# Kernel optimization log

Hardware: AMD Instinct MI355X
Metric: run time of the kernel (lower is better)

Reference implementation:

```python
import jax, jax.numpy as jnp
import numpy as np

B, N, E = 64, 1024, 16384  # graphs, nodes per graph, edges per graph
N_ITER = 5
NORMALIZE = True
NUM_INIT_LABELS = 16


def _unique_inverse(h):
    """Equivalent of torch.unique(h, sorted=True, return_inverse=True)[1] for 1-D h."""
    order = jnp.argsort(h)
    sh = h[order]
    bnd = jnp.concatenate([jnp.zeros(1, jnp.int32), (sh[1:] != sh[:-1]).astype(jnp.int32)])
    ranks = jnp.cumsum(bnd)  # dense rank in sorted-unique order
    return jnp.zeros_like(ranks).at[order].set(ranks)


def _wl_iteration(mask, labels, hash_w):
    """One WL iteration for all graphs.
    mask: [B,N,N] bool dense adjacency (sparse-to-dense, as in the torch code)
    labels: [B,N] int32
    hash_w: [2] float32 (Linear(2,1,bias=False) weight)
    Returns new labels [B,N] int32.
    """
    w0, w1 = hash_w[0], hash_w[1]
    lab_f = labels.astype(jnp.float32)
    deg = mask.sum(-1).astype(jnp.float32)                      # [B,N] valid-neighbor count
    K = deg.max(axis=-1, keepdims=True)                         # per-graph max_neighbors
    # sum of neighbor labels (gather+reduce over the dense mask, memory-bound)
    seg = jnp.einsum('bij,bj->bi', mask.astype(jnp.float32), lab_f)  # [B,N]
    # torch builds [N,max_neighbors] rows: node label in col 0-feature, sorted
    # neighbor labels (padded with -1) in col 1-feature, hashes each pair with
    # w0*node + w1*neigh and sums over columns. Closed form (sort is sum-invariant):
    #   K*w0*node + w1*(sum_neighbors - (K - deg))
    hashed = K * w0 * lab_f + w1 * (seg + deg - K)              # [B,N]
    return jax.vmap(_unique_inverse)(hashed)


def setup_inputs() -> dict:
    key = jax.random.key(0)
    k1, k2, k3, k4 = jax.random.split(key, 4)
    edge_src = jax.random.randint(k1, (B, E), 0, N, dtype=jnp.int32)
    edge_dst = jax.random.randint(k2, (B, E), 0, N, dtype=jnp.int32)
    labels = jax.random.randint(k3, (B, N), 0, NUM_INIT_LABELS, dtype=jnp.int32)
    hash_w = jax.random.normal(k4, (2,), dtype=jnp.float32)
    return {"edge_src": edge_src, "edge_dst": edge_dst, "labels": labels, "hash_w": hash_w}


def reference(edge_src, edge_dst, labels, hash_w):
    # sparse-to-dense neighbor mask, as in the torch module
    b_idx = jnp.arange(B, dtype=jnp.int32)[:, None]
    mask = jnp.zeros((B, N, N), dtype=bool).at[b_idx, edge_src, edge_dst].set(True)

    all_labels = [labels]
    for _ in range(N_ITER):
        all_labels.append(_wl_iteration(mask, all_labels[-1], hash_w))

    # feature vectors: per graph, bincount of labels summed over all iterations.
    # Labels are always < N (unique-inverse ranks < N; initial labels < 16),
    # so N bins is a tight static upper bound for torch's max_label+1; the extra
    # zero columns do not change the Gram matrix.
    labels_all = jnp.stack(all_labels, axis=1).reshape(B, -1)   # [B, (n_iter+1)*N]
    feats = jax.vmap(lambda l: jnp.zeros((N,), jnp.float32).at[l].add(1.0))(labels_all)

    kernel = feats @ feats.T                                    # [B,B]
    if NORMALIZE:
        d = jnp.sqrt(jnp.diag(kernel))
        kernel = kernel / (d[None, :] * d[:, None])
    return kernel
```

## Files before the change

### kernel.cpp

```cpp
#include <hip/hip_runtime.h>

#define B 64
#define N 1024
#define E 16384
#define WPR 32
#define NITER 5
#define CSR_SLOTS (E + N)
#define MAXP 20

#define FEATS_OFF 0
#define DIAG_OFF  ((size_t)B * N * 4)

__global__ void __launch_bounds__(1024) wl_mega_k(const int* __restrict__ src,
                                                  const int* __restrict__ dstp,
                                                  const int* __restrict__ lab0,
                                                  const float* __restrict__ hw,
                                                  unsigned int* __restrict__ feats,
                                                  float* __restrict__ diag) {
    __shared__ union {
        unsigned int chunk[N * WPR];
        struct {
            unsigned short nbr[CSR_SLOTS];
            struct {
                int hist[N];
                int scan[N];
                float grp[N];
                int flag[N];
            } pb;
            int meta[N];
            unsigned short perm[N];
            int dh[256];
            int dtop[256];
        } s;
    } u;
    __shared__ int s_lab[N + 2];
    __shared__ unsigned int s_feats[N];
    __shared__ int s_wsum[16];
    __shared__ int s_kp[16];
    __shared__ float s_mn[16], s_mx[16];
    __shared__ int s_anytie;
    int b = blockIdx.x, t = threadIdx.x;
    int lane = t & 63, w = t >> 6;

    const int* sg = src + (size_t)b * E;
    const int* dg_ = dstp + (size_t)b * E;
    int es[16], ed[16];
#pragma unroll
    for (int k = 0; k < 16; ++k) {
        es[k] = sg[t + k * 1024];
        ed[k] = dg_[t + k * 1024];
    }
    int l0 = lab0[(size_t)b * N + t];
    float w0 = hw[0], w1 = hw[1];
#pragma unroll
    for (int k = 0; k < 8; ++k)
        ((uint4*)u.chunk)[t + k * 1024] = make_uint4(0, 0, 0, 0);
    s_lab[t] = l0;
    s_feats[t] = 0;
    if (t == 0) { s_lab[N] = 0; s_anytie = 0; }
    __syncthreads();
#pragma unroll
    for (int v = 0; v < 16; ++v) {
        unsigned long long m = __ballot(l0 == v);
        if (lane == v) {
            int c = __popcll(m);
            if (c) atomicAdd(&s_feats[v], (unsigned)c);
        }
    }

#pragma unroll
    for (int k = 0; k < 16; ++k) {
        int wlog = ed[k] >> 5;
        int g = wlog >> 2;
        int p = (g + es[k]) & 7;
        atomicOr(&u.chunk[es[k] * WPR + p * 4 + (wlog & 3)], 1u << (ed[k] & 31));
    }
    __syncthreads();
    uint4 r[8];
    {
        const uint4* row4 = (const uint4*)(u.chunk + t * WPR);
#pragma unroll
        for (int g = 0; g < 8; ++g)
            r[g] = row4[(g + t) & 7];
    }
    __syncthreads();

    int dg = 0;
#pragma unroll
    for (int k = 0; k < 8; ++k)
        dg += __popc(r[k].x) + __popc(r[k].y) + __popc(r[k].z) + __popc(r[k].w);
    int alloc = (dg + 1) & ~1;

    int f = alloc;
#pragma unroll
    for (int d2 = 1; d2 < 64; d2 <<= 1) {
        int v = __shfl_up(f, d2);
        if (lane >= d2) f += v;
    }
    int km = dg;
#pragma unroll
    for (int o = 32; o > 0; o >>= 1) km = max(km, __shfl_down(km, o));
    if (lane == 63) s_wsum[w] = f;
    if (lane == 0)  s_kp[w] = km;
    __syncthreads();
    float Kf;
    int start;
    {
        int vv = ((lane & 15) < w) ? s_wsum[lane & 15] : 0;
#pragma unroll
        for (int m2 = 1; m2 < 16; m2 <<= 1) vv += __shfl_xor(vv, m2);
        start = (f - alloc) + vv;
        int kk = s_kp[lane & 15];
#pragma unroll
        for (int m2 = 8; m2 >= 1; m2 >>= 1) kk = max(kk, __shfl_xor(kk, m2));
        Kf = (float)kk;
    }
    u.s.pb.hist[t] = 0;
    u.s.pb.flag[t] = 0;
    if (t < 256) u.s.dh[t] = 0;

    {
        int idx = start;
#pragma unroll
        for (int k = 0; k < 8; ++k) {
            unsigned int wv[4] = { r[k].x, r[k].y, r[k].z, r[k].w };
#pragma unroll
            for (int c2 = 0; c2 < 4; ++c2) {
                unsigned int word = wv[c2];
                int bb = (k * 4 + c2) << 5;
                while (word) {
                    int j = __ffs(word) - 1;
                    word &= word - 1;
                    u.s.nbr[idx++] = (unsigned short)(bb + j);
                }
            }
        }
        if (dg & 1) u.s.nbr[idx] = (unsigned short)N;
    }
    u.s.meta[t] = (start << 11) | dg;
    __syncthreads();

    atomicAdd(&u.s.dh[min(dg, 255)], 1);
    __syncthreads();
    if (w == 0) {
        int h0 = u.s.dh[lane * 4], h1 = u.s.dh[lane * 4 + 1];
        int h2 = u.s.dh[lane * 4 + 2], h3 = u.s.dh[lane * 4 + 3];
        int c1 = h0 + h1, c2 = c1 + h2, c3 = c2 + h3;
        int ex = c3;
#pragma unroll
        for (int d2 = 1; d2 < 64; d2 <<= 1) {
            int v = __shfl_up(ex, d2);
            if (lane >= d2) ex += v;
        }
        ex -= c3;
        u.s.dtop[lane * 4]     = N - (ex + h0);
        u.s.dtop[lane * 4 + 1] = N - (ex + c1);
        u.s.dtop[lane * 4 + 2] = N - (ex + c2);
        u.s.dtop[lane * 4 + 3] = N - (ex + c3);
    }
    __syncthreads();
    {
        int pos = atomicAdd(&u.s.dtop[min(dg, 255)], 1);
        u.s.perm[pos] = (unsigned short)t;
    }
    __syncthreads();
    int v_node = u.s.perm[t];
    int mv = u.s.meta[v_node];
    int vdeg = mv & 2047;
    int vpstart = (mv >> 11) >> 1;
    int vpairs = ((vdeg + 1) & ~1) >> 1;
    int lab_reg = s_lab[v_node];
    const unsigned int* nbr32 = (const unsigned int*)u.s.nbr;
    unsigned int pw[MAXP];
#pragma unroll
    for (int k = 0; k < MAXP; ++k) {
        unsigned int pk = 0u;
        if (k < vpairs) pk = nbr32[vpstart + k];
        pw[k] = pk;
    }

    int nfast = 0;
    for (int it = 0; it < NITER; ++it) {
        int ssum = 0;
#pragma unroll
        for (int k = 0; k < MAXP; ++k) if (k < vpairs) {
            unsigned int pr = pw[k];
            ssum += s_lab[pr & 0xFFFFu] + s_lab[pr >> 16];
        }
        for (int k = MAXP; k < vpairs; ++k) {
            unsigned int pr = nbr32[vpstart + k];
            ssum += s_lab[pr & 0xFFFFu] + s_lab[pr >> 16];
        }
        float t1 = __fmul_rn(__fmul_rn(Kf, w0), (float)lab_reg);
        float t2 = __fmul_rn(w1, __fsub_rn(__fadd_rn((float)ssum, (float)vdeg), Kf));
        float h  = __fadd_rn(t1, t2);

        float mn = h, mx = h;
#pragma unroll
        for (int o = 32; o > 0; o >>= 1) {
            mn = fminf(mn, __shfl_down(mn, o));
            mx = fmaxf(mx, __shfl_down(mx, o));
        }
        if (lane == 0) { s_mn[w] = mn; s_mx[w] = mx; }
        __syncthreads();
        float fmn, span;
        {
            float a = s_mn[lane & 15];
            float cmx = s_mx[lane & 15];
#pragma unroll
            for (int m2 = 8; m2 >= 1; m2 >>= 1) {
                a = fminf(a, __shfl_xor(a, m2));
                cmx = fmaxf(cmx, __shfl_xor(cmx, m2));
            }
            fmn = a;
            span = cmx - a;
        }
        float scale = (span > 0.f) ? (1023.0f / span) : 0.f;
        int bucket = min((int)((h - fmn) * scale), 1023);
        int off_in = atomicAdd(&u.s.pb.hist[bucket], 1);
        __syncthreads();

        f = u.s.pb.hist[t];
#pragma unroll
        for (int d2 = 1; d2 < 64; d2 <<= 1) {
            int v = __shfl_up(f, d2);
            if (lane >= d2) f += v;
        }
        if (lane == 63) s_wsum[w] = f;
        __syncthreads();
        {
            int vv = ((lane & 15) < w) ? s_wsum[lane & 15] : 0;
#pragma unroll
            for (int m2 = 1; m2 < 16; m2 <<= 1) vv += __shfl_xor(vv, m2);
            u.s.pb.scan[t] = f + vv;
        }
        __syncthreads();

        int bs = u.s.pb.scan[bucket] - u.s.pb.hist[bucket];
        int be = u.s.pb.scan[bucket];
        u.s.pb.grp[bs + off_in] = h;
        __syncthreads();

        int cr = bs;
        int eq = 0;
        for (int k = bs; k < be; ++k) {
            float g = u.s.pb.grp[k];
            cr += (g < h);
            eq += (g == h);
        }
        if (eq > 1) s_anytie = it + 1;
        u.s.pb.hist[t] = 0;
        __syncthreads();

        if (s_anytie != it + 1) {
            s_lab[v_node] = cr;
            lab_reg = cr;
            ++nfast;
        } else {
            u.s.pb.flag[cr] = 1;
            __syncthreads();
            int f2 = u.s.pb.flag[t];
#pragma unroll
            for (int d2 = 1; d2 < 64; d2 <<= 1) {
                int v = __shfl_up(f2, d2);
                if (lane >= d2) f2 += v;
            }
            if (lane == 63) s_wsum[w] = f2;
            __syncthreads();
            {
                int vv = ((lane & 15) < w) ? s_wsum[lane & 15] : 0;
#pragma unroll
                for (int m2 = 1; m2 < 16; m2 <<= 1) vv += __shfl_xor(vv, m2);
                u.s.pb.scan[t] = f2 + vv;
            }
            u.s.pb.flag[t] = 0;
            __syncthreads();
            int rank = u.s.pb.scan[cr] - 1;
            s_lab[v_node] = rank;
            lab_reg = rank;
            atomicAdd(&s_feats[rank], 1u);
        }
        __syncthreads();
    }

    unsigned int fv = s_feats[t] + (unsigned)nfast;
    feats[(size_t)b * N + t] = fv;
    int sq = (int)(fv * fv);
#pragma unroll
    for (int o = 32; o > 0; o >>= 1) sq += __shfl_down(sq, o);
    if (lane == 0) s_wsum[w] = sq;
    __syncthreads();
    if (t == 0) {
        int tot = 0;
#pragma unroll
        for (int k = 0; k < 16; ++k) tot += s_wsum[k];
        diag[b] = (float)tot;
    }
}

__global__ void __launch_bounds__(256) gram_k(const unsigned int* __restrict__ feats,
                                              const float* __restrict__ diag,
                                              float* __restrict__ out) {
    __shared__ unsigned int s_fi[N];
    int i = blockIdx.x, t = threadIdx.x;
    int lane = t & 63, w = t >> 6;
    ((uint4*)s_fi)[t] = ((const uint4*)(feats + (size_t)i * N))[t];
    __syncthreads();
    float di = diag[i];
    for (int jj = 0; jj < 16; ++jj) {
        int j = w * 16 + jj;
        const uint4* fj = (const uint4*)(feats + (size_t)j * N);
        const uint4* fi = (const uint4*)s_fi;
        int s = 0;
#pragma unroll
        for (int k = 0; k < 4; ++k) {
            uint4 vb = fj[lane + k * 64];
            uint4 va = fi[lane + k * 64];
            s += (int)(va.x * vb.x) + (int)(va.y * vb.y)
               + (int)(va.z * vb.z) + (int)(va.w * vb.w);
        }
#pragma unroll
        for (int off = 32; off > 0; off >>= 1) s += __shfl_down(s, off);
        if (lane == 0) out[i * B + j] = (float)s / sqrtf(di * diag[j]);
    }
}

extern "C" void kernel_launch(void* const* d_in, const int* in_sizes, int n_in,
                              void* d_out, int out_size, void* d_ws, size_t ws_size,
                              hipStream_t stream) {
    const int*   esrc = (const int*)d_in[0];
    const int*   edst = (const int*)d_in[1];
    const int*   lab0 = (const int*)d_in[2];
    const float* hw   = (const float*)d_in[3];

    char* ws = (char*)d_ws;
    unsigned int* feats = (unsigned int*)(ws + FEATS_OFF);
    float*        diag  = (float*)(ws + DIAG_OFF);

    wl_mega_k<<<B, 1024, 0, stream>>>(esrc, edst, lab0, hw, feats, diag);
    gram_k<<<B, 256, 0, stream>>>(feats, diag, (float*)d_out);
}
```

Before: 104.9 us.

## Drop degree-sorted node permutation, pad neighbor pairs with sentinel, widen gram kernel

Removes the degree-histogram counting sort that permuted nodes across threads, so each thread now processes its own node directly. This drops several barriers and atomics during setup. Neighbor pairs beyond the degree are padded with a sentinel pair pointing at a spare label slot, which makes the unrolled gather branch-free. The fast path no longer needs an extra barrier after the tie check. The gram kernel now uses 1024 threads per block, so each wave handles 4 columns instead of 16. The trade-off is lost load balancing: without the degree sort, high-degree nodes can share a wave with low-degree ones and cause divergence in the gather loop.

```diff
diff --git a/kernel.cpp b/kernel.cpp
--- a/kernel.cpp
+++ b/kernel.cpp
@@ -7,6 +7,7 @@
 #define NITER 5
 #define CSR_SLOTS (E + N)
 #define MAXP 20
+#define SENT_PAIR 0x04000400u
 
 #define FEATS_OFF 0
 #define DIAG_OFF  ((size_t)B * N * 4)
@@ -27,10 +28,6 @@
                 float grp[N];
                 int flag[N];
             } pb;
-            int meta[N];
-            unsigned short perm[N];
-            int dh[256];
-            int dtop[256];
         } s;
     } u;
     __shared__ int s_lab[N + 2];
@@ -117,7 +114,6 @@
     }
     u.s.pb.hist[t] = 0;
     u.s.pb.flag[t] = 0;
-    if (t < 256) u.s.dh[t] = 0;
 
     {
         int idx = start;
@@ -137,53 +133,23 @@
         }
         if (dg & 1) u.s.nbr[idx] = (unsigned short)N;
     }
-    u.s.meta[t] = (start << 11) | dg;
-    __syncthreads();
-
-    atomicAdd(&u.s.dh[min(dg, 255)], 1);
-    __syncthreads();
-    if (w == 0) {
-        int h0 = u.s.dh[lane * 4], h1 = u.s.dh[lane * 4 + 1];
-        int h2 = u.s.dh[lane * 4 + 2], h3 = u.s.dh[lane * 4 + 3];
-        int c1 = h0 + h1, c2 = c1 + h2, c3 = c2 + h3;
-        int ex = c3;
-#pragma unroll
-        for (int d2 = 1; d2 < 64; d2 <<= 1) {
-            int v = __shfl_up(ex, d2);
-            if (lane >= d2) ex += v;
-        }
-        ex -= c3;
-        u.s.dtop[lane * 4]     = N - (ex + h0);
-        u.s.dtop[lane * 4 + 1] = N - (ex + c1);
-        u.s.dtop[lane * 4 + 2] = N - (ex + c2);
-        u.s.dtop[lane * 4 + 3] = N - (ex + c3);
-    }
-    __syncthreads();
-    {
-        int pos = atomicAdd(&u.s.dtop[min(dg, 255)], 1);
-        u.s.perm[pos] = (unsigned short)t;
-    }
-    __syncthreads();
-    int v_node = u.s.perm[t];
-    int mv = u.s.meta[v_node];
-    int vdeg = mv & 2047;
-    int vpstart = (mv >> 11) >> 1;
-    int vpairs = ((vdeg + 1) & ~1) >> 1;
-    int lab_reg = s_lab[v_node];
+    __syncthreads();
+
+    int vdeg = dg;
+    int vpstart = start >> 1;
+    int vpairs = alloc >> 1;
+    int lab_reg = l0;
     const unsigned int* nbr32 = (const unsigned int*)u.s.nbr;
     unsigned int pw[MAXP];
 #pragma unroll
-    for (int k = 0; k < MAXP; ++k) {
-        unsigned int pk = 0u;
-        if (k < vpairs) pk = nbr32[vpstart + k];
-        pw[k] = pk;
-    }
+    for (int k = 0; k < MAXP; ++k)
+        pw[k] = (k < vpairs) ? nbr32[vpstart + k] : SENT_PAIR;
 
     int nfast = 0;
     for (int it = 0; it < NITER; ++it) {
         int ssum = 0;
 #pragma unroll
-        for (int k = 0; k < MAXP; ++k) if (k < vpairs) {
+        for (int k = 0; k < MAXP; ++k) {
             unsigned int pr = pw[k];
             ssum += s_lab[pr & 0xFFFFu] + s_lab[pr >> 16];
         }
@@ -250,13 +216,9 @@
         }
         if (eq > 1) s_anytie = it + 1;
         u.s.pb.hist[t] = 0;
-        __syncthreads();
-
-        if (s_anytie != it + 1) {
-            s_lab[v_node] = cr;
-            lab_reg = cr;
-            ++nfast;
-        } else {
+        s_lab[t] = cr;
+        __syncthreads();
+        if (s_anytie == it + 1) {
             u.s.pb.flag[cr] = 1;
             __syncthreads();
             int f2 = u.s.pb.flag[t];
@@ -276,11 +238,14 @@
             u.s.pb.flag[t] = 0;
             __syncthreads();
             int rank = u.s.pb.scan[cr] - 1;
-            s_lab[v_node] = rank;
+            s_lab[t] = rank;
             lab_reg = rank;
             atomicAdd(&s_feats[rank], 1u);
-        }
-        __syncthreads();
+            __syncthreads();
+        } else {
+            lab_reg = cr;
+            ++nfast;
+        }
     }
 
     unsigned int fv = s_feats[t] + (unsigned)nfast;
@@ -298,17 +263,19 @@
     }
 }
 
-__global__ void __launch_bounds__(256) gram_k(const unsigned int* __restrict__ feats,
-                                              const float* __restrict__ diag,
-                                              float* __restrict__ out) {
+__global__ void __launch_bounds__(1024) gram_k(const unsigned int* __restrict__ feats,
+                                               const float* __restrict__ diag,
+                                               float* __restrict__ out) {
     __shared__ unsigned int s_fi[N];
     int i = blockIdx.x, t = threadIdx.x;
     int lane = t & 63, w = t >> 6;
-    ((uint4*)s_fi)[t] = ((const uint4*)(feats + (size_t)i * N))[t];
+    if (t < 256)
+        ((uint4*)s_fi)[t] = ((const uint4*)(feats + (size_t)i * N))[t];
     __syncthreads();
     float di = diag[i];
-    for (int jj = 0; jj < 16; ++jj) {
-        int j = w * 16 + jj;
+#pragma unroll
+    for (int jj = 0; jj < 4; ++jj) {
+        int j = w * 4 + jj;
         const uint4* fj = (const uint4*)(feats + (size_t)j * N);
         const uint4* fi = (const uint4*)s_fi;
         int s = 0;
@@ -338,5 +305,5 @@
     float*        diag  = (float*)(ws + DIAG_OFF);
 
     wl_mega_k<<<B, 1024, 0, stream>>>(esrc, edst, lab0, hw, feats, diag);
-    gram_k<<<B, 256, 0, stream>>>(feats, diag, (float*)d_out);
+    gram_k<<<B, 1024, 0, stream>>>(feats, diag, (float*)d_out);
 }
```

New measurement: 99.25 us. 1.06x faster.

## Fold degree sort into setup, trim barriers, wave-uniform neighbor loop, wider gram

Applied to the files above, without the earlier changes.

The degree histogram atomics move earlier and keep their returned slot, so the permutation position comes from the scanned top-of-bucket plus that slot. This drops two barriers and a second round of atomics. The neighbor-pair loop now runs in chunks of four, bounded by the wave-wide maximum pair count and padded with sentinel pairs, which removes per-element divergent predicates. In the fast path (no ties) the per-iteration trailing barrier is dropped, and the Gram kernel uses 1024 threads with 4 columns per wave instead of 16. The barrier removal depends on the label write and the anytie flag being ordered correctly across iterations, which carries some race risk.

```diff
diff --git a/kernel.cpp b/kernel.cpp
--- a/kernel.cpp
+++ b/kernel.cpp
@@ -7,6 +7,7 @@
 #define NITER 5
 #define CSR_SLOTS (E + N)
 #define MAXP 20
+#define SENT_PAIR 0x04000400u
 
 #define FEATS_OFF 0
 #define DIAG_OFF  ((size_t)B * N * 4)
@@ -29,8 +30,6 @@
             } pb;
             int meta[N];
             unsigned short perm[N];
-            int dh[256];
-            int dtop[256];
         } s;
     } u;
     __shared__ int s_lab[N + 2];
@@ -39,6 +38,8 @@
     __shared__ int s_kp[16];
     __shared__ float s_mn[16], s_mx[16];
     __shared__ int s_anytie;
+    __shared__ int s_dh[256];
+    __shared__ int s_dtop[256];
     int b = blockIdx.x, t = threadIdx.x;
     int lane = t & 63, w = t >> 6;
 
@@ -57,6 +58,7 @@
         ((uint4*)u.chunk)[t + k * 1024] = make_uint4(0, 0, 0, 0);
     s_lab[t] = l0;
     s_feats[t] = 0;
+    if (t < 256) s_dh[t] = 0;
     if (t == 0) { s_lab[N] = 0; s_anytie = 0; }
     __syncthreads();
 #pragma unroll
@@ -89,6 +91,8 @@
 #pragma unroll
     for (int k = 0; k < 8; ++k)
         dg += __popc(r[k].x) + __popc(r[k].y) + __popc(r[k].z) + __popc(r[k].w);
+    int dbin = min(dg, 255);
+    int pib = atomicAdd(&s_dh[dbin], 1);
     int alloc = (dg + 1) & ~1;
 
     int f = alloc;
@@ -115,9 +119,24 @@
         for (int m2 = 8; m2 >= 1; m2 >>= 1) kk = max(kk, __shfl_xor(kk, m2));
         Kf = (float)kk;
     }
+    if (w == 0) {
+        int h0 = s_dh[lane * 4], h1 = s_dh[lane * 4 + 1];
+        int h2 = s_dh[lane * 4 + 2], h3 = s_dh[lane * 4 + 3];
+        int c1 = h0 + h1, c2 = c1 + h2, c3 = c2 + h3;
+        int ex = c3;
+#pragma unroll
+        for (int d2 = 1; d2 < 64; d2 <<= 1) {
+            int v = __shfl_up(ex, d2);
+            if (lane >= d2) ex += v;
+        }
+        ex -= c3;
+        s_dtop[lane * 4]     = N - (ex + h0);
+        s_dtop[lane * 4 + 1] = N - (ex + c1);
+        s_dtop[lane * 4 + 2] = N - (ex + c2);
+        s_dtop[lane * 4 + 3] = N - (ex + c3);
+    }
     u.s.pb.hist[t] = 0;
     u.s.pb.flag[t] = 0;
-    if (t < 256) u.s.dh[t] = 0;
 
     {
         int idx = start;
@@ -140,52 +159,50 @@
     u.s.meta[t] = (start << 11) | dg;
     __syncthreads();
 
-    atomicAdd(&u.s.dh[min(dg, 255)], 1);
-    __syncthreads();
-    if (w == 0) {
-        int h0 = u.s.dh[lane * 4], h1 = u.s.dh[lane * 4 + 1];
-        int h2 = u.s.dh[lane * 4 + 2], h3 = u.s.dh[lane * 4 + 3];
-        int c1 = h0 + h1, c2 = c1 + h2, c3 = c2 + h3;
-        int ex = c3;
-#pragma unroll
-        for (int d2 = 1; d2 < 64; d2 <<= 1) {
-            int v = __shfl_up(ex, d2);
-            if (lane >= d2) ex += v;
-        }
-        ex -= c3;
-        u.s.dtop[lane * 4]     = N - (ex + h0);
-        u.s.dtop[lane * 4 + 1] = N - (ex + c1);
-        u.s.dtop[lane * 4 + 2] = N - (ex + c2);
-        u.s.dtop[lane * 4 + 3] = N - (ex + c3);
-    }
-    __syncthreads();
     {
-        int pos = atomicAdd(&u.s.dtop[min(dg, 255)], 1);
+        int pos = s_dtop[dbin] + pib;
         u.s.perm[pos] = (unsigned short)t;
     }
     __syncthreads();
+
     int v_node = u.s.perm[t];
     int mv = u.s.meta[v_node];
     int vdeg = mv & 2047;
     int vpstart = (mv >> 11) >> 1;
-    int vpairs = ((vdeg + 1) & ~1) >> 1;
+    int vpairs = (((mv & 2047) + 1) & ~1) >> 1;
     int lab_reg = s_lab[v_node];
     const unsigned int* nbr32 = (const unsigned int*)u.s.nbr;
+    int wmax = vpairs;
+#pragma unroll
+    for (int m2 = 32; m2 >= 1; m2 >>= 1) wmax = max(wmax, __shfl_xor(wmax, m2));
+    wmax = __builtin_amdgcn_readfirstlane(wmax);
     unsigned int pw[MAXP];
 #pragma unroll
-    for (int k = 0; k < MAXP; ++k) {
-        unsigned int pk = 0u;
-        if (k < vpairs) pk = nbr32[vpstart + k];
-        pw[k] = pk;
+    for (int c = 0; c < MAXP / 4; ++c) {
+        if (c * 4 < wmax) {
+#pragma unroll
+            for (int k = 0; k < 4; ++k) {
+                int kk = c * 4 + k;
+                pw[kk] = (kk < vpairs) ? nbr32[vpstart + kk] : SENT_PAIR;
+            }
+        } else {
+#pragma unroll
+            for (int k = 0; k < 4; ++k) pw[c * 4 + k] = SENT_PAIR;
+        }
     }
 
     int nfast = 0;
     for (int it = 0; it < NITER; ++it) {
         int ssum = 0;
 #pragma unroll
-        for (int k = 0; k < MAXP; ++k) if (k < vpairs) {
-            unsigned int pr = pw[k];
-            ssum += s_lab[pr & 0xFFFFu] + s_lab[pr >> 16];
+        for (int c = 0; c < MAXP / 4; ++c) {
+            if (c * 4 < wmax) {
+#pragma unroll
+                for (int k = 0; k < 4; ++k) {
+                    unsigned int pr = pw[c * 4 + k];
+                    ssum += s_lab[pr & 0xFFFFu] + s_lab[pr >> 16];
+                }
+            }
         }
         for (int k = MAXP; k < vpairs; ++k) {
             unsigned int pr = nbr32[vpstart + k];
@@ -250,13 +267,9 @@
         }
         if (eq > 1) s_anytie = it + 1;
         u.s.pb.hist[t] = 0;
-        __syncthreads();
-
-        if (s_anytie != it + 1) {
-            s_lab[v_node] = cr;
-            lab_reg = cr;
-            ++nfast;
-        } else {
+        s_lab[v_node] = cr;
+        __syncthreads();
+        if (s_anytie == it + 1) {
             u.s.pb.flag[cr] = 1;
             __syncthreads();
             int f2 = u.s.pb.flag[t];
@@ -279,8 +292,11 @@
             s_lab[v_node] = rank;
             lab_reg = rank;
             atomicAdd(&s_feats[rank], 1u);
-        }
-        __syncthreads();
+            __syncthreads();
+        } else {
+            lab_reg = cr;
+            ++nfast;
+        }
     }
 
     unsigned int fv = s_feats[t] + (unsigned)nfast;
@@ -298,17 +314,19 @@
     }
 }
 
-__global__ void __launch_bounds__(256) gram_k(const unsigned int* __restrict__ feats,
-                                              const float* __restrict__ diag,
-                                              float* __restrict__ out) {
+__global__ void __launch_bounds__(1024) gram_k(const unsigned int* __restrict__ feats,
+                                               const float* __restrict__ diag,
+                                               float* __restrict__ out) {
     __shared__ unsigned int s_fi[N];
     int i = blockIdx.x, t = threadIdx.x;
     int lane = t & 63, w = t >> 6;
-    ((uint4*)s_fi)[t] = ((const uint4*)(feats + (size_t)i * N))[t];
+    if (t < 256)
+        ((uint4*)s_fi)[t] = ((const uint4*)(feats + (size_t)i * N))[t];
     __syncthreads();
     float di = diag[i];
-    for (int jj = 0; jj < 16; ++jj) {
-        int j = w * 16 + jj;
+#pragma unroll
+    for (int jj = 0; jj < 4; ++jj) {
+        int j = w * 4 + jj;
         const uint4* fj = (const uint4*)(feats + (size_t)j * N);
         const uint4* fi = (const uint4*)s_fi;
         int s = 0;
@@ -338,5 +356,5 @@
     float*        diag  = (float*)(ws + DIAG_OFF);
 
     wl_mega_k<<<B, 1024, 0, stream>>>(esrc, edst, lab0, hw, feats, diag);
-    gram_k<<<B, 256, 0, stream>>>(feats, diag, (float*)d_out);
+    gram_k<<<B, 1024, 0, stream>>>(feats, diag, (float*)d_out);
 }
```

Result: faster. 98.85 us (-5.8%).
